# Kernel optimization log

Measured on AMD Instinct MI355X. Metric: run time of the kernel, lower is better.

## Reference

```python
import jax, jax.numpy as jnp
import numpy as np

N = 200_000      # nodes
E = 1_000_000    # edges
B = 4096         # source batch
K = 20           # n_neighbors
DN = 128         # n_node_features
DEMB = 128       # embedding_dimension (interval emb hidden)
DMEM = DN + DEMB # memory dim (forced by memory + cat(node_feat, delta_emb))
DT = 128         # n_time_features
DE = 128         # n_edge_features
NBINS = 300


def setup_inputs() -> dict:
    key = jax.random.key(0)
    ks = jax.random.split(key, 16)
    return {
        "node_features": jax.random.normal(ks[0], (N, DN), jnp.float32),
        "edge_features": jax.random.normal(ks[1], (E, DE), jnp.float32),
        "memory": jax.random.normal(ks[2], (N, DMEM), jnp.float32),
        "interval_table": jax.random.normal(ks[3], (NBINS, DEMB), jnp.float32),
        "bin_boundaries": jnp.linspace(0.0, 100.0, NBINS + 1).astype(jnp.float32),
        "time_w": jax.random.normal(ks[4], (DT,), jnp.float32),
        "time_b": jax.random.normal(ks[5], (DT,), jnp.float32),
        "W_agg": jax.random.normal(ks[6], (DT + DE, DMEM), jnp.float32) / np.sqrt(DT + DE),
        "timestamps": jax.random.uniform(ks[7], (B,), jnp.float32, 0.0, 100.0),
        "edge_times": jax.random.uniform(ks[8], (B, K), jnp.float32, 0.0, 100.0),
        "intervals": jax.random.uniform(ks[9], (B,), jnp.float32, 0.0, 100.0),
        "nei_intervals": jax.random.uniform(ks[10], (B, K), jnp.float32, 0.0, 100.0),
        "source_nodes": jax.random.randint(ks[11], (B,), 0, N),
        "neighbors": jax.random.randint(ks[12], (B, K), 0, N),
        "edge_idxs": jax.random.randint(ks[13], (B, K), 0, E),
    }


def reference(node_features, edge_features, memory, interval_table, bin_boundaries,
              time_w, time_b, W_agg, timestamps, edge_times, intervals,
              nei_intervals, source_nodes, neighbors, edge_idxs):
    # LearnableIntervalEmbedding.forward: bucketize -> clamp -> embedding lookup
    def interval_embed(x):
        idx = jnp.searchsorted(bin_boundaries, x, side='left') - 1  # torch.bucketize(right=False)
        idx = jnp.clip(idx, 0, NBINS - 1)
        return interval_table[idx]

    # TGN-style time encoder: cos(t * w + b)
    def time_enc(t):
        return jnp.cos(t[..., None] * time_w + time_b)

    # n_layers == 0 path: memory add + gather + interval embed + concat
    def layer0(idx, ivals):
        return memory[idx] + jnp.concatenate(
            [node_features[idx], interval_embed(ivals)], axis=-1)

    src0 = layer0(source_nodes, intervals)          # [B, DMEM]
    nb0 = layer0(neighbors, nei_intervals)          # [B, K, DMEM]

    edge_deltas = timestamps[:, None] - edge_times  # [B, K]
    ete = time_enc(edge_deltas)                     # [B, K, DT]
    ef = edge_features[edge_idxs]                   # [B, K, DE]
    # aggregate (abstract in source): masked mean of neighbor embeddings plus
    # linearly merged (edge_time_emb, edge_feat) messages, added to source emb.
    msg = jnp.einsum('bkf,fd->bkd', jnp.concatenate([ete, ef], axis=-1), W_agg)

    valid = (neighbors != -1)[..., None].astype(src0.dtype)  # mask = neighbors == -1
    cnt = jnp.maximum(valid.sum(axis=1), 1.0)
    out = src0 + (nb0 * valid).sum(axis=1) / cnt + (msg * valid).sum(axis=1) / cnt
    return out
```

## Files before the change

kernel.cpp:

```cpp
#include <hip/hip_runtime.h>
#include <math.h>

#define KN     20
#define DMEMC  256
#define DNC    128
#define DTC    128
#define DEC    128
#define DEMBC  128
#define NBINSC 300
#define MPB    4

__global__ __launch_bounds__(256) void graph_emb_kernel(
    const float* __restrict__ node_features,
    const float* __restrict__ edge_features,
    const float* __restrict__ memory_,
    const float* __restrict__ interval_table,
    const float* __restrict__ bin_boundaries,
    const float* __restrict__ time_w,
    const float* __restrict__ time_b,
    const float* __restrict__ W_agg,
    const float* __restrict__ timestamps,
    const float* __restrict__ edge_times,
    const float* __restrict__ intervals,
    const float* __restrict__ nei_intervals,
    const int*   __restrict__ source_nodes,
    const int*   __restrict__ neighbors,
    const int*   __restrict__ edge_idxs,
    float* __restrict__ out, int B)
{
    __shared__ float s_bb[NBINSC + 1];
    __shared__ float s_feat[MPB][DMEMC];
    __shared__ int   s_bins[MPB][KN + 1];

    const int t  = threadIdx.x;
    const int b0 = blockIdx.x * MPB;

    for (int i = t; i < NBINSC + 1; i += 256) s_bb[i] = bin_boundaries[i];
    __syncthreads();

    if (t < MPB * (KN + 1)) {
        const int m = t / (KN + 1), j = t % (KN + 1);
        const int b = b0 + m;
        const float x = (j == 0) ? intervals[b] : nei_intervals[b * KN + (j - 1)];
        int lo = 0, hi = NBINSC + 1;
        while (lo < hi) {
            int mid = (lo + hi) >> 1;
            if (s_bb[mid] < x) lo = mid + 1; else hi = mid;
        }
        int idx = lo - 1;
        idx = idx < 0 ? 0 : (idx > NBINSC - 1 ? NBINSC - 1 : idx);
        s_bins[m][j] = idx;
    }

    #pragma unroll
    for (int m = 0; m < MPB; ++m) {
        const int b = b0 + m;
        float fs = 0.f;
        if (t < DTC) {
            const float tsv = timestamps[b];
            const float w = time_w[t], bc = time_b[t];
            #pragma unroll
            for (int k = 0; k < KN; ++k) {
                if (neighbors[b * KN + k] != -1) {
                    const float delta = tsv - edge_times[b * KN + k];
                    fs += cosf(fmaf(delta, w, bc));
                }
            }
        } else {
            const int d = t - DTC;
            #pragma unroll
            for (int k = 0; k < KN; ++k) {
                if (neighbors[b * KN + k] != -1) {
                    const int e = edge_idxs[b * KN + k];
                    fs += edge_features[e * DEC + d];
                }
            }
        }
        s_feat[m][t] = fs;
    }
    __syncthreads();

    float res[MPB];
    float cnt_m[MPB];
    #pragma unroll
    for (int m = 0; m < MPB; ++m) {
        const int b = b0 + m;
        const int src = source_nodes[b];
        float v = memory_[src * DMEMC + t];
        if (t < DNC) v += node_features[src * DNC + t];
        else         v += interval_table[s_bins[m][0] * DEMBC + (t - DNC)];

        float nbacc = 0.f;
        float cnt = 0.f;
        #pragma unroll
        for (int k = 0; k < KN; ++k) {
            const int nb = neighbors[b * KN + k];
            if (nb != -1) {
                cnt += 1.f;
                float x = memory_[nb * DMEMC + t];
                if (t < DNC) x += node_features[nb * DNC + t];
                else         x += interval_table[s_bins[m][k + 1] * DEMBC + (t - DNC)];
                nbacc += x;
            }
        }
        cnt = fmaxf(cnt, 1.f);
        cnt_m[m] = cnt;
        res[m] = v + nbacc / cnt;
    }

    float acc[MPB] = {0.f, 0.f, 0.f, 0.f};
    for (int f = 0; f < DMEMC; ++f) {
        const float w = W_agg[f * DMEMC + t];
        #pragma unroll
        for (int m = 0; m < MPB; ++m) acc[m] += s_feat[m][f] * w;
    }

    #pragma unroll
    for (int m = 0; m < MPB; ++m) {
        out[(b0 + m) * DMEMC + t] = res[m] + acc[m] / cnt_m[m];
    }
}

extern "C" void kernel_launch(void* const* d_in, const int* in_sizes, int n_in,
                              void* d_out, int out_size, void* d_ws, size_t ws_size,
                              hipStream_t stream) {
    const float* node_features  = (const float*)d_in[0];
    const float* edge_features  = (const float*)d_in[1];
    const float* memory_        = (const float*)d_in[2];
    const float* interval_table = (const float*)d_in[3];
    const float* bin_boundaries = (const float*)d_in[4];
    const float* time_w         = (const float*)d_in[5];
    const float* time_b         = (const float*)d_in[6];
    const float* W_agg          = (const float*)d_in[7];
    const float* timestamps     = (const float*)d_in[8];
    const float* edge_times     = (const float*)d_in[9];
    const float* intervals      = (const float*)d_in[10];
    const float* nei_intervals  = (const float*)d_in[11];
    const int*   source_nodes   = (const int*)d_in[12];
    const int*   neighbors      = (const int*)d_in[13];
    const int*   edge_idxs      = (const int*)d_in[14];
    float* out = (float*)d_out;

    const int B = in_sizes[8];
    const int grid = (B + MPB - 1) / MPB;
    graph_emb_kernel<<<grid, 256, 0, stream>>>(
        node_features, edge_features, memory_, interval_table, bin_boundaries,
        time_w, time_b, W_agg, timestamps, edge_times, intervals, nei_intervals,
        source_nodes, neighbors, edge_idxs, out, B);
}
```

Before: 779.7 us.

## Map one wavefront per batch row with float4 gathers and fast cosine

Each 64-lane wavefront now handles one batch row. Every lane loads float4 slices of the memory, node-feature, interval and edge-feature rows, where before every thread did scalar loads for each of the four rows. Partial results go through shared memory, and the time encoding uses __cosf instead of cosf. The aim is fewer memory instructions and more memory-level parallelism for the gathers. The trade-offs are an extra shared buffer and lower cosine accuracy for large arguments.

Measured after the change: 743.3 us. 4.7% less time.

```diff
diff --git a/kernel.cpp b/kernel.cpp
--- a/kernel.cpp
+++ b/kernel.cpp
@@ -4,11 +4,14 @@
 #define KN     20
 #define DMEMC  256
 #define DNC    128
-#define DTC    128
 #define DEC    128
 #define DEMBC  128
 #define NBINSC 300
 #define MPB    4
+
+__device__ __forceinline__ float4 ld4(const float* p) {
+    return *reinterpret_cast<const float4*>(p);
+}
 
 __global__ __launch_bounds__(256) void graph_emb_kernel(
     const float* __restrict__ node_features,
@@ -29,19 +32,21 @@
     float* __restrict__ out, int B)
 {
     __shared__ float s_bb[NBINSC + 1];
-    __shared__ float s_feat[MPB][DMEMC];
-    __shared__ int   s_bins[MPB][KN + 1];
+    __shared__ __align__(16) float s_feat[MPB][DMEMC];
+    __shared__ __align__(16) float s_res[MPB][DMEMC];
+    __shared__ int s_bins[MPB][KN + 1];
 
     const int t  = threadIdx.x;
+    const int w  = t >> 6;
+    const int l  = t & 63;
     const int b0 = blockIdx.x * MPB;
+    const int b  = b0 + w;
 
-    for (int i = t; i < NBINSC + 1; i += 256) s_bb[i] = bin_boundaries[i];
+    for (int i = t; i <= NBINSC; i += 256) s_bb[i] = bin_boundaries[i];
     __syncthreads();
 
-    if (t < MPB * (KN + 1)) {
-        const int m = t / (KN + 1), j = t % (KN + 1);
-        const int b = b0 + m;
-        const float x = (j == 0) ? intervals[b] : nei_intervals[b * KN + (j - 1)];
+    if (l <= KN && b < B) {
+        const float x = (l == 0) ? intervals[b] : nei_intervals[b * KN + (l - 1)];
         int lo = 0, hi = NBINSC + 1;
         while (lo < hi) {
             int mid = (lo + hi) >> 1;
@@ -49,76 +54,87 @@
         }
         int idx = lo - 1;
         idx = idx < 0 ? 0 : (idx > NBINSC - 1 ? NBINSC - 1 : idx);
-        s_bins[m][j] = idx;
-    }
-
-    #pragma unroll
-    for (int m = 0; m < MPB; ++m) {
-        const int b = b0 + m;
-        float fs = 0.f;
-        if (t < DTC) {
-            const float tsv = timestamps[b];
-            const float w = time_w[t], bc = time_b[t];
-            #pragma unroll
-            for (int k = 0; k < KN; ++k) {
-                if (neighbors[b * KN + k] != -1) {
-                    const float delta = tsv - edge_times[b * KN + k];
-                    fs += cosf(fmaf(delta, w, bc));
-                }
-            }
-        } else {
-            const int d = t - DTC;
-            #pragma unroll
-            for (int k = 0; k < KN; ++k) {
-                if (neighbors[b * KN + k] != -1) {
-                    const int e = edge_idxs[b * KN + k];
-                    fs += edge_features[e * DEC + d];
-                }
-            }
-        }
-        s_feat[m][t] = fs;
+        s_bins[w][l] = idx;
     }
     __syncthreads();
 
-    float res[MPB];
-    float cnt_m[MPB];
-    #pragma unroll
-    for (int m = 0; m < MPB; ++m) {
-        const int b = b0 + m;
-        const int src = source_nodes[b];
-        float v = memory_[src * DMEMC + t];
-        if (t < DNC) v += node_features[src * DNC + t];
-        else         v += interval_table[s_bins[m][0] * DEMBC + (t - DNC)];
+    if (b < B) {
+        float cnt = 0.f;
+        #pragma unroll
+        for (int k = 0; k < KN; ++k) cnt += (neighbors[b * KN + k] != -1) ? 1.f : 0.f;
+        const float inv = 1.f / fmaxf(cnt, 1.f);
 
-        float nbacc = 0.f;
-        float cnt = 0.f;
+        const int d0 = 4 * l;
+
+        const long src = source_nodes[b];
+        float4 v = ld4(memory_ + src * DMEMC + d0);
+        if (l < 32) {
+            float4 a = ld4(node_features + src * DNC + d0);
+            v.x += a.x; v.y += a.y; v.z += a.z; v.w += a.w;
+        } else {
+            float4 a = ld4(interval_table + (long)s_bins[w][0] * DEMBC + (d0 - 128));
+            v.x += a.x; v.y += a.y; v.z += a.z; v.w += a.w;
+        }
+        float4 nb4 = make_float4(0.f, 0.f, 0.f, 0.f);
         #pragma unroll
         for (int k = 0; k < KN; ++k) {
             const int nb = neighbors[b * KN + k];
             if (nb != -1) {
-                cnt += 1.f;
-                float x = memory_[nb * DMEMC + t];
-                if (t < DNC) x += node_features[nb * DNC + t];
-                else         x += interval_table[s_bins[m][k + 1] * DEMBC + (t - DNC)];
-                nbacc += x;
+                float4 x = ld4(memory_ + (long)nb * DMEMC + d0);
+                float4 a;
+                if (l < 32) a = ld4(node_features + (long)nb * DNC + d0);
+                else        a = ld4(interval_table + (long)s_bins[w][k + 1] * DEMBC + (d0 - 128));
+                nb4.x += x.x + a.x; nb4.y += x.y + a.y;
+                nb4.z += x.z + a.z; nb4.w += x.w + a.w;
             }
         }
-        cnt = fmaxf(cnt, 1.f);
-        cnt_m[m] = cnt;
-        res[m] = v + nbacc / cnt;
+        float4 r = make_float4(v.x + nb4.x * inv, v.y + nb4.y * inv,
+                               v.z + nb4.z * inv, v.w + nb4.w * inv);
+        *reinterpret_cast<float4*>(&s_res[w][d0]) = r;
+
+        float4 fs = make_float4(0.f, 0.f, 0.f, 0.f);
+        if (l < 32) {
+            const float4 w4 = ld4(time_w + d0);
+            const float4 c4 = ld4(time_b + d0);
+            const float ts = timestamps[b];
+            #pragma unroll
+            for (int k = 0; k < KN; ++k) {
+                if (neighbors[b * KN + k] != -1) {
+                    const float dlt = ts - edge_times[b * KN + k];
+                    fs.x += __cosf(fmaf(dlt, w4.x, c4.x));
+                    fs.y += __cosf(fmaf(dlt, w4.y, c4.y));
+                    fs.z += __cosf(fmaf(dlt, w4.z, c4.z));
+                    fs.w += __cosf(fmaf(dlt, w4.w, c4.w));
+                }
+            }
+        } else {
+            const int e0 = d0 - 128;
+            #pragma unroll
+            for (int k = 0; k < KN; ++k) {
+                if (neighbors[b * KN + k] != -1) {
+                    const long e = edge_idxs[b * KN + k];
+                    float4 a = ld4(edge_features + e * DEC + e0);
+                    fs.x += a.x; fs.y += a.y; fs.z += a.z; fs.w += a.w;
+                }
+            }
+        }
+        fs.x *= inv; fs.y *= inv; fs.z *= inv; fs.w *= inv;
+        *reinterpret_cast<float4*>(&s_feat[w][d0]) = fs;
     }
+    __syncthreads();
 
-    float acc[MPB] = {0.f, 0.f, 0.f, 0.f};
+    float a0 = 0.f, a1 = 0.f, a2 = 0.f, a3 = 0.f;
     for (int f = 0; f < DMEMC; ++f) {
-        const float w = W_agg[f * DMEMC + t];
-        #pragma unroll
-        for (int m = 0; m < MPB; ++m) acc[m] += s_feat[m][f] * w;
+        const float wv = W_agg[f * DMEMC + t];
+        a0 = fmaf(s_feat[0][f], wv, a0);
+        a1 = fmaf(s_feat[1][f], wv, a1);
+        a2 = fmaf(s_feat[2][f], wv, a2);
+        a3 = fmaf(s_feat[3][f], wv, a3);
     }
-
-    #pragma unroll
-    for (int m = 0; m < MPB; ++m) {
-        out[(b0 + m) * DMEMC + t] = res[m] + acc[m] / cnt_m[m];
-    }
+    if (b0 + 0 < B) out[(long)(b0 + 0) * DMEMC + t] = s_res[0][t] + a0;
+    if (b0 + 1 < B) out[(long)(b0 + 1) * DMEMC + t] = s_res[1][t] + a1;
+    if (b0 + 2 < B) out[(long)(b0 + 2) * DMEMC + t] = s_res[2][t] + a2;
+    if (b0 + 3 < B) out[(long)(b0 + 3) * DMEMC + t] = s_res[3][t] + a3;
 }
 
 extern "C" void kernel_launch(void* const* d_in, const int* in_sizes, int n_in,
```
